# Optimization experiments

Hardware: AMD Instinct MI355X
Metric: run time of the kernel (lower is better)

## Reference

```python
import jax, jax.numpy as jnp
import numpy as np

EPS = 1e-05

def setup_inputs() -> dict:
    key = jax.random.key(0)
    N, U = 131072, 256  # n_features (total nodes), n_units
    x = jax.random.normal(key, (N, U), dtype=jnp.float32)
    gamma = jnp.ones((N, U), dtype=jnp.float32)
    beta = jnp.ones((N, U), dtype=jnp.float32)
    return {"x": x, "gamma": gamma, "beta": beta, "batch_size": 64}

def reference(x, gamma, beta, batch_size):
    N, U = x.shape
    n = N // batch_size  # nodes per graph (tf.split into equal chunks)
    xr = x.reshape(batch_size, n, U)
    mean = jnp.mean(xr, axis=1, keepdims=True)            # per-graph, per-unit mean
    std = jnp.std(xr, axis=1, keepdims=True)              # population std (ddof=0), as tf.reduce_std
    xn = ((xr - mean) / (std + EPS)).reshape(N, U)
    return gamma * xn + beta
```

## Files before the change

### kernel.cpp

```cpp
#include <hip/hip_runtime.h>

#define GN_EPS 1e-5f

typedef float f32x4 __attribute__((ext_vector_type(4)));

constexpr int U       = 256;
constexpr int NPG     = 2048;
constexpr int NGRAPH  = 64;
constexpr int UF4     = U / 4;

constexpr int CH      = 32;
constexpr int RPC     = NPG / CH;
constexpr int K1_BLK  = 256;
constexpr int K1_WAVES = K1_BLK / 64;
constexpr int K1_ITERS = RPC / K1_WAVES;

constexpr int CH3     = 64;
constexpr int RPC3    = NPG / CH3;
constexpr int K3_BLK  = 256;
constexpr int K3_ITERS = (RPC3 * UF4) / K3_BLK;

constexpr size_t WS_SUM_OFF  = 0;
constexpr size_t WS_SQ_OFF   = (size_t)NGRAPH * CH * U;
constexpr size_t WS_MEAN_OFF = WS_SQ_OFF + (size_t)NGRAPH * CH * U;
constexpr size_t WS_INV_OFF  = WS_MEAN_OFF + (size_t)NGRAPH * U;

__global__ __launch_bounds__(K1_BLK) void gn_partial(
    const float* __restrict__ x, float* __restrict__ ws)
{
    const int chunk = blockIdx.x & (CH - 1);
    const int graph = blockIdx.x / CH;
    const int t     = threadIdx.x;
    const int wave  = t >> 6;
    const int lane  = t & 63;

    const size_t row0 = (size_t)graph * NPG + (size_t)chunk * RPC + wave;
    const f32x4* xr = reinterpret_cast<const f32x4*>(x) + row0 * UF4 + lane;

    f32x4 s = (f32x4)0.f;
    f32x4 q = (f32x4)0.f;
#pragma unroll 8
    for (int i = 0; i < K1_ITERS; ++i) {
        const f32x4 v = xr[(size_t)i * K1_WAVES * UF4];
        s += v;
        q += v * v;
    }

    __shared__ f32x4 ssum[K1_WAVES][64];
    __shared__ f32x4 ssq [K1_WAVES][64];
    ssum[wave][lane] = s;
    ssq [wave][lane] = q;
    __syncthreads();

    if (t < 64) {
        f32x4 s2 = ssum[0][t];
        f32x4 q2 = ssq [0][t];
#pragma unroll
        for (int w = 1; w < K1_WAVES; ++w) {
            s2 += ssum[w][t];
            q2 += ssq [w][t];
        }
        const size_t o = ((size_t)graph * CH + chunk) * UF4 + t;
        reinterpret_cast<f32x4*>(ws + WS_SUM_OFF)[o] = s2;
        reinterpret_cast<f32x4*>(ws + WS_SQ_OFF )[o] = q2;
    }
}

__global__ __launch_bounds__(U) void gn_finalize(float* __restrict__ ws)
{
    const int graph = blockIdx.x;
    const int t     = threadIdx.x;

    const float* psum = ws + WS_SUM_OFF + (size_t)graph * CH * U + t;
    const float* psq  = ws + WS_SQ_OFF  + (size_t)graph * CH * U + t;
    float s = 0.f, q = 0.f;
#pragma unroll
    for (int c = 0; c < CH; ++c) {
        s += psum[(size_t)c * U];
        q += psq [(size_t)c * U];
    }
    const float invn = 1.0f / (float)NPG;
    const float mean = s * invn;
    const float var  = fmaxf(q * invn - mean * mean, 0.f);
    ws[WS_MEAN_OFF + (size_t)graph * U + t] = mean;
    ws[WS_INV_OFF  + (size_t)graph * U + t] = 1.0f / (sqrtf(var) + GN_EPS);
}

__global__ __launch_bounds__(K3_BLK) void gn_normalize(
    const float* __restrict__ x,
    const float* __restrict__ gamma,
    const float* __restrict__ beta,
    const float* __restrict__ ws,
    float* __restrict__ out)
{
    const int chunk = blockIdx.x & (CH3 - 1);
    const int graph = blockIdx.x / CH3;
    const int t     = threadIdx.x;

    const int f4 = t & (UF4 - 1);
    const f32x4 m  = reinterpret_cast<const f32x4*>(ws + WS_MEAN_OFF + (size_t)graph * U)[f4];
    const f32x4 iv = reinterpret_cast<const f32x4*>(ws + WS_INV_OFF  + (size_t)graph * U)[f4];

    const size_t f4base = ((size_t)graph * NPG + (size_t)chunk * RPC3) * UF4;
    const f32x4* xv = reinterpret_cast<const f32x4*>(x)     + f4base;
    const f32x4* gv = reinterpret_cast<const f32x4*>(gamma) + f4base;
    const f32x4* bv = reinterpret_cast<const f32x4*>(beta)  + f4base;
    f32x4*       ov = reinterpret_cast<f32x4*>(out)         + f4base;

#pragma unroll 4
    for (int i = 0; i < K3_ITERS; ++i) {
        const int idx = i * K3_BLK + t;
        const f32x4 v  = xv[idx];
        const f32x4 g4 = __builtin_nontemporal_load(gv + idx);
        const f32x4 b4 = __builtin_nontemporal_load(bv + idx);
        const f32x4 o  = g4 * ((v - m) * iv) + b4;
        __builtin_nontemporal_store(o, ov + idx);
    }
}

extern "C" void kernel_launch(void* const* d_in, const int* in_sizes, int n_in,
                              void* d_out, int out_size, void* d_ws, size_t ws_size,
                              hipStream_t stream) {
    const float* x     = (const float*)d_in[0];
    const float* gamma = (const float*)d_in[1];
    const float* beta  = (const float*)d_in[2];
    float* out = (float*)d_out;
    float* ws  = (float*)d_ws;
    (void)in_sizes; (void)n_in; (void)out_size; (void)ws_size;

    gn_partial  <<<NGRAPH * CH,  K1_BLK, 0, stream>>>(x, ws);
    gn_finalize <<<NGRAPH,       U,      0, stream>>>(ws);
    gn_normalize<<<NGRAPH * CH3, K3_BLK, 0, stream>>>(x, gamma, beta, ws, out);
}
```

Baseline: 402.0 us.

## Fuse partial, finalize and normalize into one cooperative grid-synced kernel

Merges the three launches into a single cooperative kernel with two grid-wide barriers. The same block re-reads the x chunk it just reduced, which may still hit in cache, and the finalize step is spread across all blocks using a wavefront shuffle reduction. Falls back to the three-kernel path if the cooperative launch fails. The risks are grid-sync overhead and 2048 blocks needing to be co-resident (launch bounds of 8 blocks per CU); the normalize chunking also changes from 64 to 32 chunks per graph.

```diff
diff --git a/kernel.cpp b/kernel.cpp
--- a/kernel.cpp
+++ b/kernel.cpp
@@ -1,4 +1,7 @@
 #include <hip/hip_runtime.h>
+#include <hip/hip_cooperative_groups.h>
+
+namespace cg = cooperative_groups;
 
 #define GN_EPS 1e-5f
 
@@ -11,43 +14,44 @@
 
 constexpr int CH      = 32;
 constexpr int RPC     = NPG / CH;
-constexpr int K1_BLK  = 256;
-constexpr int K1_WAVES = K1_BLK / 64;
-constexpr int K1_ITERS = RPC / K1_WAVES;
-
-constexpr int CH3     = 64;
-constexpr int RPC3    = NPG / CH3;
-constexpr int K3_BLK  = 256;
-constexpr int K3_ITERS = (RPC3 * UF4) / K3_BLK;
-
-constexpr size_t WS_SUM_OFF  = 0;
-constexpr size_t WS_SQ_OFF   = (size_t)NGRAPH * CH * U;
-constexpr size_t WS_MEAN_OFF = WS_SQ_OFF + (size_t)NGRAPH * CH * U;
-constexpr size_t WS_INV_OFF  = WS_MEAN_OFF + (size_t)NGRAPH * U;
-
-__global__ __launch_bounds__(K1_BLK) void gn_partial(
-    const float* __restrict__ x, float* __restrict__ ws)
-{
-    const int chunk = blockIdx.x & (CH - 1);
-    const int graph = blockIdx.x / CH;
-    const int t     = threadIdx.x;
-    const int wave  = t >> 6;
-    const int lane  = t & 63;
-
-    const size_t row0 = (size_t)graph * NPG + (size_t)chunk * RPC + wave;
+constexpr int BLK     = 256;
+constexpr int WAVES   = BLK / 64;
+constexpr int NBLK    = NGRAPH * CH;
+constexpr int A_ITERS = RPC / WAVES;
+constexpr int B_ITERS = RPC * UF4 / BLK;
+
+constexpr size_t WS_SUM  = 0;
+constexpr size_t WS_SQ   = (size_t)NGRAPH * CH * U;
+constexpr size_t WS_MEAN = WS_SQ + (size_t)NGRAPH * CH * U;
+constexpr size_t WS_INV  = WS_MEAN + (size_t)NGRAPH * U;
+
+__global__ __launch_bounds__(BLK, 8) void gn_fused(
+    const float* __restrict__ x,
+    const float* __restrict__ gamma,
+    const float* __restrict__ beta,
+    float* __restrict__ ws,
+    float* __restrict__ out)
+{
+    const int bid  = blockIdx.x;
+    const int c    = bid & (CH - 1);
+    const int g    = bid / CH;
+    const int t    = threadIdx.x;
+    const int wave = t >> 6;
+    const int lane = t & 63;
+
+    const size_t row0 = (size_t)g * NPG + (size_t)c * RPC + wave;
     const f32x4* xr = reinterpret_cast<const f32x4*>(x) + row0 * UF4 + lane;
-
     f32x4 s = (f32x4)0.f;
     f32x4 q = (f32x4)0.f;
 #pragma unroll 8
-    for (int i = 0; i < K1_ITERS; ++i) {
-        const f32x4 v = xr[(size_t)i * K1_WAVES * UF4];
+    for (int i = 0; i < A_ITERS; ++i) {
+        const f32x4 v = xr[(size_t)i * WAVES * UF4];
         s += v;
         q += v * v;
     }
 
-    __shared__ f32x4 ssum[K1_WAVES][64];
-    __shared__ f32x4 ssq [K1_WAVES][64];
+    __shared__ f32x4 ssum[WAVES][64];
+    __shared__ f32x4 ssq [WAVES][64];
     ssum[wave][lane] = s;
     ssq [wave][lane] = q;
     __syncthreads();
@@ -56,60 +60,121 @@
         f32x4 s2 = ssum[0][t];
         f32x4 q2 = ssq [0][t];
 #pragma unroll
-        for (int w = 1; w < K1_WAVES; ++w) {
-            s2 += ssum[w][t];
-            q2 += ssq [w][t];
+        for (int w = 1; w < WAVES; ++w) { s2 += ssum[w][t]; q2 += ssq[w][t]; }
+        const size_t o = ((size_t)g * CH + c) * UF4 + t;
+        reinterpret_cast<f32x4*>(ws + WS_SUM)[o] = s2;
+        reinterpret_cast<f32x4*>(ws + WS_SQ )[o] = q2;
+    }
+
+    cg::this_grid().sync();
+
+    {
+        const int c2 = t & 31;
+        const int ul = t >> 5;
+        const int u  = c * 8 + ul;
+        float ps = ws[WS_SUM + ((size_t)g * CH + c2) * U + u];
+        float pq = ws[WS_SQ  + ((size_t)g * CH + c2) * U + u];
+#pragma unroll
+        for (int m = 1; m < 32; m <<= 1) {
+            ps += __shfl_xor(ps, m);
+            pq += __shfl_xor(pq, m);
         }
-        const size_t o = ((size_t)graph * CH + chunk) * UF4 + t;
-        reinterpret_cast<f32x4*>(ws + WS_SUM_OFF)[o] = s2;
-        reinterpret_cast<f32x4*>(ws + WS_SQ_OFF )[o] = q2;
+        if (c2 == 0) {
+            const float invn = 1.0f / (float)NPG;
+            const float mean = ps * invn;
+            const float var  = fmaxf(pq * invn - mean * mean, 0.f);
+            ws[WS_MEAN + (size_t)g * U + u] = mean;
+            ws[WS_INV  + (size_t)g * U + u] = 1.0f / (sqrtf(var) + GN_EPS);
+        }
+    }
+
+    cg::this_grid().sync();
+
+    const int f4 = t & (UF4 - 1);
+    const f32x4 m  = reinterpret_cast<const f32x4*>(ws + WS_MEAN + (size_t)g * U)[f4];
+    const f32x4 iv = reinterpret_cast<const f32x4*>(ws + WS_INV  + (size_t)g * U)[f4];
+
+    const size_t base = ((size_t)g * NPG + (size_t)c * RPC) * UF4;
+    const f32x4* xv = reinterpret_cast<const f32x4*>(x)     + base;
+    const f32x4* gv = reinterpret_cast<const f32x4*>(gamma) + base;
+    const f32x4* bv = reinterpret_cast<const f32x4*>(beta)  + base;
+    f32x4*       ov = reinterpret_cast<f32x4*>(out)         + base;
+
+#pragma unroll 4
+    for (int i = 0; i < B_ITERS; ++i) {
+        const int idx = i * BLK + t;
+        const f32x4 v  = xv[idx];
+        const f32x4 g4 = __builtin_nontemporal_load(gv + idx);
+        const f32x4 b4 = __builtin_nontemporal_load(bv + idx);
+        const f32x4 o  = g4 * ((v - m) * iv) + b4;
+        __builtin_nontemporal_store(o, ov + idx);
+    }
+}
+
+__global__ __launch_bounds__(BLK) void gn_partial(
+    const float* __restrict__ x, float* __restrict__ ws)
+{
+    const int c = blockIdx.x & (CH - 1);
+    const int g = blockIdx.x / CH;
+    const int t = threadIdx.x;
+    const int wave = t >> 6, lane = t & 63;
+    const size_t row0 = (size_t)g * NPG + (size_t)c * RPC + wave;
+    const f32x4* xr = reinterpret_cast<const f32x4*>(x) + row0 * UF4 + lane;
+    f32x4 s = (f32x4)0.f, q = (f32x4)0.f;
+#pragma unroll 8
+    for (int i = 0; i < A_ITERS; ++i) {
+        const f32x4 v = xr[(size_t)i * WAVES * UF4];
+        s += v; q += v * v;
+    }
+    __shared__ f32x4 ssum[WAVES][64];
+    __shared__ f32x4 ssq [WAVES][64];
+    ssum[wave][lane] = s; ssq[wave][lane] = q;
+    __syncthreads();
+    if (t < 64) {
+        f32x4 s2 = ssum[0][t], q2 = ssq[0][t];
+#pragma unroll
+        for (int w = 1; w < WAVES; ++w) { s2 += ssum[w][t]; q2 += ssq[w][t]; }
+        const size_t o = ((size_t)g * CH + c) * UF4 + t;
+        reinterpret_cast<f32x4*>(ws + WS_SUM)[o] = s2;
+        reinterpret_cast<f32x4*>(ws + WS_SQ )[o] = q2;
     }
 }
 
 __global__ __launch_bounds__(U) void gn_finalize(float* __restrict__ ws)
 {
-    const int graph = blockIdx.x;
-    const int t     = threadIdx.x;
-
-    const float* psum = ws + WS_SUM_OFF + (size_t)graph * CH * U + t;
-    const float* psq  = ws + WS_SQ_OFF  + (size_t)graph * CH * U + t;
+    const int g = blockIdx.x;
+    const int t = threadIdx.x;
+    const float* psum = ws + WS_SUM + (size_t)g * CH * U + t;
+    const float* psq  = ws + WS_SQ  + (size_t)g * CH * U + t;
     float s = 0.f, q = 0.f;
 #pragma unroll
-    for (int c = 0; c < CH; ++c) {
-        s += psum[(size_t)c * U];
-        q += psq [(size_t)c * U];
-    }
+    for (int c = 0; c < CH; ++c) { s += psum[(size_t)c * U]; q += psq[(size_t)c * U]; }
     const float invn = 1.0f / (float)NPG;
     const float mean = s * invn;
     const float var  = fmaxf(q * invn - mean * mean, 0.f);
-    ws[WS_MEAN_OFF + (size_t)graph * U + t] = mean;
-    ws[WS_INV_OFF  + (size_t)graph * U + t] = 1.0f / (sqrtf(var) + GN_EPS);
-}
-
-__global__ __launch_bounds__(K3_BLK) void gn_normalize(
-    const float* __restrict__ x,
-    const float* __restrict__ gamma,
-    const float* __restrict__ beta,
-    const float* __restrict__ ws,
+    ws[WS_MEAN + (size_t)g * U + t] = mean;
+    ws[WS_INV  + (size_t)g * U + t] = 1.0f / (sqrtf(var) + GN_EPS);
+}
+
+__global__ __launch_bounds__(BLK) void gn_normalize(
+    const float* __restrict__ x, const float* __restrict__ gamma,
+    const float* __restrict__ beta, const float* __restrict__ ws,
     float* __restrict__ out)
 {
-    const int chunk = blockIdx.x & (CH3 - 1);
-    const int graph = blockIdx.x / CH3;
-    const int t     = threadIdx.x;
-
+    const int c = blockIdx.x & (CH - 1);
+    const int g = blockIdx.x / CH;
+    const int t = threadIdx.x;
     const int f4 = t & (UF4 - 1);
-    const f32x4 m  = reinterpret_cast<const f32x4*>(ws + WS_MEAN_OFF + (size_t)graph * U)[f4];
-    const f32x4 iv = reinterpret_cast<const f32x4*>(ws + WS_INV_OFF  + (size_t)graph * U)[f4];
-
-    const size_t f4base = ((size_t)graph * NPG + (size_t)chunk * RPC3) * UF4;
-    const f32x4* xv = reinterpret_cast<const f32x4*>(x)     + f4base;
-    const f32x4* gv = reinterpret_cast<const f32x4*>(gamma) + f4base;
-    const f32x4* bv = reinterpret_cast<const f32x4*>(beta)  + f4base;
-    f32x4*       ov = reinterpret_cast<f32x4*>(out)         + f4base;
-
+    const f32x4 m  = reinterpret_cast<const f32x4*>(ws + WS_MEAN + (size_t)g * U)[f4];
+    const f32x4 iv = reinterpret_cast<const f32x4*>(ws + WS_INV  + (size_t)g * U)[f4];
+    const size_t base = ((size_t)g * NPG + (size_t)c * RPC) * UF4;
+    const f32x4* xv = reinterpret_cast<const f32x4*>(x)     + base;
+    const f32x4* gv = reinterpret_cast<const f32x4*>(gamma) + base;
+    const f32x4* bv = reinterpret_cast<const f32x4*>(beta)  + base;
+    f32x4*       ov = reinterpret_cast<f32x4*>(out)         + base;
 #pragma unroll 4
-    for (int i = 0; i < K3_ITERS; ++i) {
-        const int idx = i * K3_BLK + t;
+    for (int i = 0; i < B_ITERS; ++i) {
+        const int idx = i * BLK + t;
         const f32x4 v  = xv[idx];
         const f32x4 g4 = __builtin_nontemporal_load(gv + idx);
         const f32x4 b4 = __builtin_nontemporal_load(bv + idx);
@@ -128,7 +193,13 @@
     float* ws  = (float*)d_ws;
     (void)in_sizes; (void)n_in; (void)out_size; (void)ws_size;
 
-    gn_partial  <<<NGRAPH * CH,  K1_BLK, 0, stream>>>(x, ws);
-    gn_finalize <<<NGRAPH,       U,      0, stream>>>(ws);
-    gn_normalize<<<NGRAPH * CH3, K3_BLK, 0, stream>>>(x, gamma, beta, ws, out);
-}
+    void* args[] = { (void*)&x, (void*)&gamma, (void*)&beta, (void*)&ws, (void*)&out };
+    hipError_t e = hipLaunchCooperativeKernel((const void*)gn_fused,
+                                              dim3(NBLK), dim3(BLK),
+                                              args, 0, stream);
+    if (e != hipSuccess) {
+        gn_partial  <<<NBLK,       BLK, 0, stream>>>(x, ws);
+        gn_finalize <<<NGRAPH,     U,   0, stream>>>(ws);
+        gn_normalize<<<NBLK,       BLK, 0, stream>>>(x, gamma, beta, ws, out);
+    }
+}
```

Result: slower. 802.6 us (+99.6%).
